# Kernel optimization log

Measured on AMD Instinct MI355X. Metric: run time of the kernel, lower is better.

The kernel has to match this reference:

```python
import jax, jax.numpy as jnp
import numpy as np

C = 512
NUM_GROUPS = 32
EPS = 1e-6


def setup_inputs() -> dict:
    key = jax.random.key(0)
    ks = jax.random.split(key, 10)
    B, H, W = 4, 64, 64
    scale = 1.0 / np.sqrt(C)
    return {
        "hidden_states": jax.random.normal(ks[0], (B, C, H, W), dtype=jnp.float32),
        "gn_scale": jnp.ones((C,), dtype=jnp.float32),
        "gn_bias": jnp.zeros((C,), dtype=jnp.float32),
        "wq": jax.random.normal(ks[1], (C, C), dtype=jnp.float32) * scale,
        "bq": jnp.zeros((C,), dtype=jnp.float32),
        "wk": jax.random.normal(ks[2], (C, C), dtype=jnp.float32) * scale,
        "bk": jnp.zeros((C,), dtype=jnp.float32),
        "wv": jax.random.normal(ks[3], (C, C), dtype=jnp.float32) * scale,
        "bv": jnp.zeros((C,), dtype=jnp.float32),
        "wp": jax.random.normal(ks[4], (C, C), dtype=jnp.float32) * scale,
        "bp": jnp.zeros((C,), dtype=jnp.float32),
    }


def _group_norm(x, scale, bias):
    # x: (B, C, H, W); GroupNorm(32 groups, eps=1e-6, affine)
    B, Cc, H, W = x.shape
    xg = x.reshape(B, NUM_GROUPS, Cc // NUM_GROUPS, H, W)
    mean = jnp.mean(xg, axis=(2, 3, 4), keepdims=True)
    var = jnp.var(xg, axis=(2, 3, 4), keepdims=True)
    xg = (xg - mean) * jax.lax.rsqrt(var + EPS)
    x = xg.reshape(B, Cc, H, W)
    return x * scale[None, :, None, None] + bias[None, :, None, None]


def _conv1x1(x, w, b):
    # 1x1 conv == channel matmul; x: (B,C,H,W), w: (Cout,Cin)
    return jnp.einsum('bchw,oc->bohw', x, w) + b[None, :, None, None]


def reference(hidden_states, gn_scale, gn_bias, wq, bq, wk, bk, wv, bv, wp, bp):
    residual = hidden_states
    h = _group_norm(hidden_states, gn_scale, gn_bias)
    q = _conv1x1(h, wq, bq)
    k = _conv1x1(h, wk, bk)
    v = _conv1x1(h, wv, bv)
    B, Cc, H, W = q.shape
    N = H * W
    q = q.reshape(B, Cc, N)  # (B,C,N)
    k = k.reshape(B, Cc, N)
    v = v.reshape(B, Cc, N)
    # attn[b,i,j] = softmax_j( q_i . k_j * C^-0.5 )
    attn = jnp.einsum('bci,bcj->bij', q, k) * (Cc ** -0.5)
    attn = jax.nn.softmax(attn, axis=2)
    # out[b,c,i] = sum_j v[b,c,j] * attn[b,i,j]
    out = jnp.einsum('bcj,bij->bci', v, attn)
    out = out.reshape(B, Cc, H, W)
    out = _conv1x1(out, wp, bp)
    return out + residual
```

## Files before the change

### kernel.cpp

```cpp
#include <hip/hip_runtime.h>
#include <cstdint>
#include <cstddef>


#define CDIM 512
#define NSP  4096
#define NB   4
#define M0   12.0f

using bf16x8 = __attribute__((ext_vector_type(8))) __bf16;
using f32x4  = __attribute__((ext_vector_type(4))) float;
using u16x4  = __attribute__((ext_vector_type(4))) unsigned short;
using h8     = __attribute__((ext_vector_type(8))) _Float16;

__device__ __forceinline__ unsigned short f2bf(float f) {
  unsigned int u = __float_as_uint(f);
  u += 0x7fffu + ((u >> 16) & 1u);
  return (unsigned short)(u >> 16);
}

__device__ __forceinline__ void async_copy16(const unsigned short* g, unsigned short* l) {
  __builtin_amdgcn_global_load_lds(
      (const __attribute__((address_space(1))) void*)g,
      (__attribute__((address_space(3))) void*)l, 16, 0, 0);
}

__global__ __launch_bounds__(256) void gn_stats(const float* __restrict__ x,
                                                float* __restrict__ stats) {
  const size_t base = (size_t)blockIdx.x * 65536;
  const float4* p = (const float4*)(x + base);
  float s = 0.f, ss = 0.f;
  for (int i = threadIdx.x; i < 16384; i += 256) {
    float4 v = p[i];
    s  += v.x + v.y + v.z + v.w;
    ss += v.x*v.x + v.y*v.y + v.z*v.z + v.w*v.w;
  }
  for (int off = 32; off; off >>= 1) {
    s  += __shfl_xor(s, off);
    ss += __shfl_xor(ss, off);
  }
  __shared__ float rs[4], rss[4];
  const int w = threadIdx.x >> 6;
  if ((threadIdx.x & 63) == 0) { rs[w] = s; rss[w] = ss; }
  __syncthreads();
  if (threadIdx.x == 0) {
    float S  = rs[0] + rs[1] + rs[2] + rs[3];
    float SS = rss[0] + rss[1] + rss[2] + rss[3];
    float mean = S * (1.f / 65536.f);
    float var  = SS * (1.f / 65536.f) - mean * mean;
    stats[2 * blockIdx.x]     = mean;
    stats[2 * blockIdx.x + 1] = rsqrtf(var + 1e-6f);
  }
}

__global__ __launch_bounds__(256) void norm_transpose(
    const float* __restrict__ x, const float* __restrict__ stats,
    const float* __restrict__ gns, const float* __restrict__ gnb,
    unsigned short* __restrict__ hnt) {
  __shared__ float tile[64][65];
  const int b  = blockIdx.z;
  const int c0 = blockIdx.y * 64, n0 = blockIdx.x * 64;
  const int tx = threadIdx.x & 63, ty = threadIdx.x >> 6;
  for (int i = 0; i < 16; ++i) {
    int cl = ty * 16 + i;
    int c  = c0 + cl;
    int g  = c >> 4;
    float mean = stats[(b * 32 + g) * 2];
    float rstd = stats[(b * 32 + g) * 2 + 1];
    float v = x[((size_t)(b * CDIM + c)) * NSP + n0 + tx];
    tile[cl][tx] = (v - mean) * rstd * gns[c] + gnb[c];
  }
  __syncthreads();
  for (int i = 0; i < 16; ++i) {
    int nl = ty * 16 + i;
    hnt[((size_t)(b * NSP + n0 + nl)) * CDIM + c0 + tx] = f2bf(tile[tx][nl]);
  }
}

__global__ __launch_bounds__(256) void weights_to_bf16(
    const float* __restrict__ w0, const float* __restrict__ w1,
    const float* __restrict__ w2, const float* __restrict__ w3,
    unsigned short* __restrict__ o0, unsigned short* __restrict__ o1,
    unsigned short* __restrict__ o2, unsigned short* __restrict__ o3) {
  const float* s; unsigned short* o;
  switch (blockIdx.y) {
    case 0: s = w0; o = o0; break;
    case 1: s = w1; o = o1; break;
    case 2: s = w2; o = o2; break;
    default: s = w3; o = o3; break;
  }
  int i = blockIdx.x * 256 + threadIdx.x;
  float4 v = ((const float4*)s)[i];
  u16x4 r = {f2bf(v.x), f2bf(v.y), f2bf(v.z), f2bf(v.w)};
  *(u16x4*)(o + (size_t)i * 4) = r;
}

template <int BIAS_MODE, int OUT_MODE, int RESID>
__global__ __launch_bounds__(256) void gemm_nt(
    const unsigned short* __restrict__ A, const unsigned short* __restrict__ Bt,
    void* __restrict__ Dv, const float* __restrict__ bias,
    const float* __restrict__ resid,
    int M, int N, int K, float scale, long sA, long sB, long sD, long sR) {
  __shared__ unsigned short lsA[2][128 * 32];
  __shared__ unsigned short lsB[2][128 * 32];
  const int tid = threadIdx.x;
  const int w = tid >> 6, lane = tid & 63;
  const int wr = w >> 1, wc = w & 1;
  const int b = blockIdx.z;
  const int bm0 = blockIdx.y * 128, bn0 = blockIdx.x * 128;
  const unsigned short* Ab = A + (size_t)b * sA;
  const unsigned short* Bb = Bt + (size_t)b * sB;

  f32x4 acc[4][4] = {};
  const int r0  = w * 16 + (lane >> 2);
  const int kof = (lane & 3) * 8;
  const int fr  = lane & 15, kf = (lane >> 4) * 8;

  for (int it = 0; it < 2; ++it) {
    int row = it * 64 + r0;
    async_copy16(Ab + (size_t)(bm0 + row) * K + kof, &lsA[0][row * 32 + kof]);
    async_copy16(Bb + (size_t)(bn0 + row) * K + kof, &lsB[0][row * 32 + kof]);
  }
  __syncthreads();

  int cur = 0;
  for (int k0 = 0; k0 < K; k0 += 32) {
    const int nk = k0 + 32;
    if (nk < K) {
      for (int it = 0; it < 2; ++it) {
        int row = it * 64 + r0;
        async_copy16(Ab + (size_t)(bm0 + row) * K + nk + kof, &lsA[cur ^ 1][row * 32 + kof]);
        async_copy16(Bb + (size_t)(bn0 + row) * K + nk + kof, &lsB[cur ^ 1][row * 32 + kof]);
      }
    }
    bf16x8 af[4], bff[4];
    for (int i = 0; i < 4; ++i) {
      af[i]  = *(const bf16x8*)(&lsA[cur][(wr * 64 + i * 16 + fr) * 32 + kf]);
      bff[i] = *(const bf16x8*)(&lsB[cur][(wc * 64 + i * 16 + fr) * 32 + kf]);
    }
    for (int i = 0; i < 4; ++i)
      for (int j = 0; j < 4; ++j)
        acc[i][j] = __builtin_amdgcn_mfma_f32_16x16x32_bf16(af[i], bff[j], acc[i][j], 0, 0, 0);
    __syncthreads();
    cur ^= 1;
  }

  const int col_l = lane & 15, row_l = (lane >> 4) * 4;
  for (int i = 0; i < 4; ++i)
    for (int j = 0; j < 4; ++j) {
      int gr = bm0 + wr * 64 + i * 16 + row_l;
      int gc = bn0 + wc * 64 + j * 16 + col_l;
      for (int r = 0; r < 4; ++r) {
        float v = acc[i][j][r] * scale;
        if (BIAS_MODE == 1) v += bias[gr + r];
        if (BIAS_MODE == 2) v += bias[gc];
        if (RESID) v += resid[(size_t)b * sR + (size_t)(gr + r) * N + gc];
        if (OUT_MODE == 1)
          ((unsigned short*)Dv)[(size_t)b * sD + (size_t)(gr + r) * N + gc] = f2bf(v);
        else
          ((float*)Dv)[(size_t)b * sD + (size_t)(gr + r) * N + gc] = v;
      }
    }
}

template <int OUT_MODE, int SPLITK, int EXPL, int XSWZ>
__global__ __launch_bounds__(256, 2) void gemm128(
    const unsigned short* __restrict__ A, const unsigned short* __restrict__ Bt,
    void* __restrict__ Dv, float* __restrict__ lsum,
    int M, int N, int K, float scale, long sA, long sB, long sD, int kLen) {
  __shared__ unsigned short lsA[2][128 * 32];
  __shared__ unsigned short lsB[2][128 * 32];
  const int tid = threadIdx.x;
  const int wid = tid >> 6, lane = tid & 63;
  const int wr = wid >> 1, wc = wid & 1;
  const int fr = lane & 15, kq = lane >> 4;
  const int b = SPLITK ? (blockIdx.z & 3) : blockIdx.z;
  int bx = blockIdx.x;
  if (XSWZ) bx = (bx & 7) * (gridDim.x >> 3) + (bx >> 3);
  const int bm0 = blockIdx.y * 128, bn0 = bx * 128;
  const unsigned short* Ab = A + (size_t)b * sA;
  const unsigned short* Bb = Bt + (size_t)b * sB;
  const size_t dOff = SPLITK ? (size_t)blockIdx.z * (size_t)M * N
                             : (size_t)b * (size_t)sD;
  const int kStart = SPLITK ? (blockIdx.z >> 2) * kLen : 0;
  const int ntiles = (SPLITK ? kLen : K) >> 5;

  auto stage = [&](int t, int buf) {
    const int k0 = kStart + t * 32;
    const int sr0 = wid * 32 + (lane >> 2);
    const int c  = lane & 3;
#pragma unroll
    for (int i = 0; i < 2; ++i) {
      const int r = sr0 + i * 16;
      async_copy16(Ab + (size_t)(bm0 + r) * K + k0 + ((c ^ (r & 3)) << 3),
                   &lsA[buf][r * 32 + c * 8]);
    }
#pragma unroll
    for (int i = 0; i < 2; ++i) {
      const int r = sr0 + i * 16;
      async_copy16(Bb + (size_t)(bn0 + r) * K + k0 + ((c ^ (r & 3)) << 3),
                   &lsB[buf][r * 32 + c * 8]);
    }
  };

  f32x4 acc[4][4] = {};
  const int cko  = (kq ^ (fr & 3)) << 3;
  const int arow = wr * 64 + fr;
  const int brow = wc * 64 + fr;

  stage(0, 0);
  for (int t = 0; t < ntiles; ++t) {
    const int cur = t & 1;
    if (t + 1 < ntiles) {
      stage(t + 1, cur ^ 1);
      asm volatile("s_waitcnt vmcnt(4)\n\ts_barrier" ::: "memory");
    } else {
      asm volatile("s_waitcnt vmcnt(0)\n\ts_barrier" ::: "memory");
    }
    bf16x8 af[4], bg[4];
#pragma unroll
    for (int i = 0; i < 4; ++i)
      af[i] = *(const bf16x8*)&lsA[cur][(arow + i * 16) * 32 + cko];
#pragma unroll
    for (int j = 0; j < 4; ++j)
      bg[j] = *(const bf16x8*)&lsB[cur][(brow + j * 16) * 32 + cko];
#pragma unroll
    for (int i = 0; i < 4; ++i)
#pragma unroll
      for (int j = 0; j < 4; ++j)
        acc[i][j] = __builtin_amdgcn_mfma_f32_16x16x32_bf16(af[i], bg[j], acc[i][j], 0, 0, 0);
    asm volatile("s_barrier" ::: "memory");
  }

  float rs[4][4];
  if (EXPL)
#pragma unroll
    for (int i = 0; i < 4; ++i)
#pragma unroll
      for (int r = 0; r < 4; ++r) rs[i][r] = 0.f;

#pragma unroll
  for (int mi = 0; mi < 4; ++mi)
#pragma unroll
    for (int ni = 0; ni < 4; ++ni) {
      const int gr = bm0 + wr * 64 + mi * 16 + kq * 4;
      const int gc = bn0 + wc * 64 + ni * 16 + fr;
#pragma unroll
      for (int r = 0; r < 4; ++r) {
        float v;
        if (EXPL) {
          v = __expf(fmaf(acc[mi][ni][r], scale, -M0));
          rs[mi][r] += v;
        } else {
          v = acc[mi][ni][r] * scale;
        }
        if (OUT_MODE == 1)
          ((unsigned short*)Dv)[dOff + (size_t)(gr + r) * N + gc] = f2bf(v);
        else
          ((_Float16*)Dv)[dOff + (size_t)(gr + r) * N + gc] = (_Float16)v;
      }
    }

  if (EXPL) {
#pragma unroll
    for (int mi = 0; mi < 4; ++mi)
#pragma unroll
      for (int r = 0; r < 4; ++r) {
        float v = rs[mi][r];
        v += __shfl_xor(v, 1); v += __shfl_xor(v, 2);
        v += __shfl_xor(v, 4); v += __shfl_xor(v, 8);
        if (fr == 0) {
          int gr = bm0 + wr * 64 + mi * 16 + kq * 4 + r;
          atomicAdd(&lsum[(size_t)b * M + gr], v);
        }
      }
  }
}

__global__ __launch_bounds__(256) void reduce_div(const _Float16* __restrict__ Op,
                                                  const float* __restrict__ l,
                                                  unsigned short* __restrict__ ot) {
  const size_t stride = (size_t)NB * NSP * CDIM;
  size_t base = ((size_t)blockIdx.x * 256 + threadIdx.x) * 8;
  float linv = 1.f / l[base >> 9];
  h8 a = *(const h8*)(Op + base);
  h8 c = *(const h8*)(Op + stride + base);
  u16x4 o0, o1;
#pragma unroll
  for (int i = 0; i < 4; ++i) {
    o0[i] = f2bf(((float)a[i] + (float)c[i]) * linv);
    o1[i] = f2bf(((float)a[i + 4] + (float)c[i + 4]) * linv);
  }
  *(u16x4*)(ot + base) = o0;
  *(u16x4*)(ot + base + 4) = o1;
}

extern "C" void kernel_launch(void* const* d_in, const int* in_sizes, int n_in,
                              void* d_out, int out_size, void* d_ws, size_t ws_size,
                              hipStream_t stream) {
  const float* hs  = (const float*)d_in[0];
  const float* gns = (const float*)d_in[1];
  const float* gnb = (const float*)d_in[2];
  const float* wq  = (const float*)d_in[3];
  const float* bq  = (const float*)d_in[4];
  const float* wk  = (const float*)d_in[5];
  const float* bk  = (const float*)d_in[6];
  const float* wv  = (const float*)d_in[7];
  const float* bv  = (const float*)d_in[8];
  const float* wp  = (const float*)d_in[9];
  const float* bp  = (const float*)d_in[10];

  char* p = (char*)d_ws;
  unsigned short* wqb = (unsigned short*)p; p += (size_t)CDIM * CDIM * 2;
  unsigned short* wkb = (unsigned short*)p; p += (size_t)CDIM * CDIM * 2;
  unsigned short* wvb = (unsigned short*)p; p += (size_t)CDIM * CDIM * 2;
  unsigned short* wpb = (unsigned short*)p; p += (size_t)CDIM * CDIM * 2;
  const size_t bn = (size_t)NSP * CDIM;
  unsigned short* hnt = (unsigned short*)p; p += NB * bn * 2;
  unsigned short* qt  = (unsigned short*)p; p += NB * bn * 2;
  unsigned short* kt  = (unsigned short*)p; p += NB * bn * 2;
  unsigned short* vcn = (unsigned short*)p; p += NB * bn * 2;
  unsigned short* P   = (unsigned short*)p; p += (size_t)NB * NSP * NSP * 2;
  _Float16* Op = (_Float16*)p;  p += (size_t)2 * NB * bn * 2;
  float* lsum  = (float*)p;     p += (size_t)NB * NSP * 4;
  float* stats = (float*)p;     p += 256 * 4;
  unsigned short* ot = hnt;

  hipMemsetAsync(lsum, 0, (size_t)NB * NSP * 4, stream);
  weights_to_bf16<<<dim3(256, 4), 256, 0, stream>>>(wq, wk, wv, wp, wqb, wkb, wvb, wpb);
  gn_stats<<<128, 256, 0, stream>>>(hs, stats);
  norm_transpose<<<dim3(64, 8, 4), 256, 0, stream>>>(hs, stats, gns, gnb, hnt);

  const long sBN = (long)bn;
  const long sPP = (long)NSP * NSP;
  gemm_nt<2, 1, 0><<<dim3(4, 32, NB), 256, 0, stream>>>(
      hnt, wqb, qt, bq, nullptr, NSP, CDIM, CDIM, 1.f, sBN, 0, sBN, 0);
  gemm_nt<2, 1, 0><<<dim3(4, 32, NB), 256, 0, stream>>>(
      hnt, wkb, kt, bk, nullptr, NSP, CDIM, CDIM, 1.f, sBN, 0, sBN, 0);
  gemm_nt<1, 1, 0><<<dim3(32, 4, NB), 256, 0, stream>>>(
      wvb, hnt, vcn, bv, nullptr, CDIM, NSP, CDIM, 1.f, 0, sBN, sBN, 0);

  const float sc = 0.044194173824159216f;
  gemm128<1, 0, 1, 1><<<dim3(32, 32, NB), 256, 0, stream>>>(
      qt, kt, P, lsum, NSP, NSP, CDIM, sc, sBN, sBN, sPP, 0);

  gemm128<2, 1, 0, 0><<<dim3(4, 32, 2 * NB), 256, 0, stream>>>(
      P, vcn, Op, nullptr, NSP, CDIM, NSP, 1.f, sPP, sBN, 0, NSP / 2);

  reduce_div<<<4096, 256, 0, stream>>>(Op, lsum, ot);

  gemm_nt<1, 0, 1><<<dim3(32, 4, NB), 256, 0, stream>>>(
      wpb, ot, (float*)d_out, bp, hs, CDIM, NSP, CDIM, 1.f, 0, sBN, sBN, sBN);
}
```

Baseline: 367.6 us.

## Enlarge attention GEMM tiles to 256x256 with 16-wave blocks and K=64 staging

Result: faster. 297.5 us (-19.1%).

```diff
diff --git a/kernel.cpp b/kernel.cpp
--- a/kernel.cpp
+++ b/kernel.cpp
@@ -163,50 +163,49 @@
     }
 }
 
-template <int OUT_MODE, int SPLITK, int EXPL, int XSWZ>
-__global__ __launch_bounds__(256, 2) void gemm128(
+template <int OUT_MODE, int SPLITK, int EXPL>
+__global__ __launch_bounds__(1024, 4) void gemm256w(
     const unsigned short* __restrict__ A, const unsigned short* __restrict__ Bt,
     void* __restrict__ Dv, float* __restrict__ lsum,
     int M, int N, int K, float scale, long sA, long sB, long sD, int kLen) {
-  __shared__ unsigned short lsA[2][128 * 32];
-  __shared__ unsigned short lsB[2][128 * 32];
+  __shared__ unsigned short lsA[2][256 * 64];
+  __shared__ unsigned short lsB[2][256 * 64];
   const int tid = threadIdx.x;
   const int wid = tid >> 6, lane = tid & 63;
-  const int wr = wid >> 1, wc = wid & 1;
+  const int wm = wid >> 2, wn = wid & 3;
   const int fr = lane & 15, kq = lane >> 4;
   const int b = SPLITK ? (blockIdx.z & 3) : blockIdx.z;
-  int bx = blockIdx.x;
-  if (XSWZ) bx = (bx & 7) * (gridDim.x >> 3) + (bx >> 3);
-  const int bm0 = blockIdx.y * 128, bn0 = bx * 128;
+  const int bm0 = blockIdx.y * 256, bn0 = blockIdx.x * 256;
   const unsigned short* Ab = A + (size_t)b * sA;
   const unsigned short* Bb = Bt + (size_t)b * sB;
   const size_t dOff = SPLITK ? (size_t)blockIdx.z * (size_t)M * N
                              : (size_t)b * (size_t)sD;
   const int kStart = SPLITK ? (blockIdx.z >> 2) * kLen : 0;
-  const int ntiles = (SPLITK ? kLen : K) >> 5;
+  const int ntiles = (SPLITK ? kLen : K) >> 6;
 
   auto stage = [&](int t, int buf) {
-    const int k0 = kStart + t * 32;
-    const int sr0 = wid * 32 + (lane >> 2);
-    const int c  = lane & 3;
+    const int k0 = kStart + t * 64;
 #pragma unroll
     for (int i = 0; i < 2; ++i) {
-      const int r = sr0 + i * 16;
-      async_copy16(Ab + (size_t)(bm0 + r) * K + k0 + ((c ^ (r & 3)) << 3),
-                   &lsA[buf][r * 32 + c * 8]);
+      const int idx = i * 1024 + tid;
+      const int row = idx >> 3, ch = idx & 7;
+      const int sch = ch ^ (row & 7);
+      async_copy16(Ab + (size_t)(bm0 + row) * K + k0 + sch * 8,
+                   &lsA[buf][row * 64 + ch * 8]);
     }
 #pragma unroll
     for (int i = 0; i < 2; ++i) {
-      const int r = sr0 + i * 16;
-      async_copy16(Bb + (size_t)(bn0 + r) * K + k0 + ((c ^ (r & 3)) << 3),
-                   &lsB[buf][r * 32 + c * 8]);
+      const int idx = i * 1024 + tid;
+      const int row = idx >> 3, ch = idx & 7;
+      const int sch = ch ^ (row & 7);
+      async_copy16(Bb + (size_t)(bn0 + row) * K + k0 + sch * 8,
+                   &lsB[buf][row * 64 + ch * 8]);
     }
   };
 
   f32x4 acc[4][4] = {};
-  const int cko  = (kq ^ (fr & 3)) << 3;
-  const int arow = wr * 64 + fr;
-  const int brow = wc * 64 + fr;
+  const int arow = wm * 64 + fr;
+  const int brow = wn * 64 + fr;
 
   stage(0, 0);
   for (int t = 0; t < ntiles; ++t) {
@@ -217,18 +216,24 @@
     } else {
       asm volatile("s_waitcnt vmcnt(0)\n\ts_barrier" ::: "memory");
     }
-    bf16x8 af[4], bg[4];
-#pragma unroll
-    for (int i = 0; i < 4; ++i)
-      af[i] = *(const bf16x8*)&lsA[cur][(arow + i * 16) * 32 + cko];
-#pragma unroll
-    for (int j = 0; j < 4; ++j)
-      bg[j] = *(const bf16x8*)&lsB[cur][(brow + j * 16) * 32 + cko];
-#pragma unroll
-    for (int i = 0; i < 4; ++i)
+    const unsigned short* la = &lsA[cur][0];
+    const unsigned short* lb = &lsB[cur][0];
+#pragma unroll
+    for (int kh = 0; kh < 2; ++kh) {
+      const int cko = ((kh * 4 + kq) ^ (fr & 7)) * 8;
+      bf16x8 af[4], bg[4];
+#pragma unroll
+      for (int i = 0; i < 4; ++i)
+        af[i] = *(const bf16x8*)&la[(arow + i * 16) * 64 + cko];
 #pragma unroll
       for (int j = 0; j < 4; ++j)
-        acc[i][j] = __builtin_amdgcn_mfma_f32_16x16x32_bf16(af[i], bg[j], acc[i][j], 0, 0, 0);
+        bg[j] = *(const bf16x8*)&lb[(brow + j * 16) * 64 + cko];
+#pragma unroll
+      for (int i = 0; i < 4; ++i)
+#pragma unroll
+        for (int j = 0; j < 4; ++j)
+          acc[i][j] = __builtin_amdgcn_mfma_f32_16x16x32_bf16(af[i], bg[j], acc[i][j], 0, 0, 0);
+    }
     asm volatile("s_barrier" ::: "memory");
   }
 
@@ -243,8 +248,8 @@
   for (int mi = 0; mi < 4; ++mi)
 #pragma unroll
     for (int ni = 0; ni < 4; ++ni) {
-      const int gr = bm0 + wr * 64 + mi * 16 + kq * 4;
-      const int gc = bn0 + wc * 64 + ni * 16 + fr;
+      const int gr = bm0 + wm * 64 + mi * 16 + kq * 4;
+      const int gc = bn0 + wn * 64 + ni * 16 + fr;
 #pragma unroll
       for (int r = 0; r < 4; ++r) {
         float v;
@@ -270,7 +275,7 @@
         v += __shfl_xor(v, 1); v += __shfl_xor(v, 2);
         v += __shfl_xor(v, 4); v += __shfl_xor(v, 8);
         if (fr == 0) {
-          int gr = bm0 + wr * 64 + mi * 16 + kq * 4 + r;
+          int gr = bm0 + wm * 64 + mi * 16 + kq * 4 + r;
           atomicAdd(&lsum[(size_t)b * M + gr], v);
         }
       }
@@ -341,10 +346,10 @@
       wvb, hnt, vcn, bv, nullptr, CDIM, NSP, CDIM, 1.f, 0, sBN, sBN, 0);
 
   const float sc = 0.044194173824159216f;
-  gemm128<1, 0, 1, 1><<<dim3(32, 32, NB), 256, 0, stream>>>(
+  gemm256w<1, 0, 1><<<dim3(16, 16, NB), 1024, 0, stream>>>(
       qt, kt, P, lsum, NSP, NSP, CDIM, sc, sBN, sBN, sPP, 0);
 
-  gemm128<2, 1, 0, 0><<<dim3(4, 32, 2 * NB), 256, 0, stream>>>(
+  gemm256w<2, 1, 0><<<dim3(2, 16, 2 * NB), 1024, 0, stream>>>(
       P, vcn, Op, nullptr, NSP, CDIM, NSP, 1.f, sPP, sBN, 0, NSP / 2);
 
   reduce_div<<<4096, 256, 0, stream>>>(Op, lsum, ot);
```

## Use 256x128 tiles with 512 threads for attention GEMMs and fuse Q/K projections

Applied to the files above, without the earlier changes.

Result: slower. 396.1 us (+7.8%).

```diff
diff --git a/kernel.cpp b/kernel.cpp
--- a/kernel.cpp
+++ b/kernel.cpp
@@ -95,18 +95,21 @@
   *(u16x4*)(o + (size_t)i * 4) = r;
 }
 
-template <int BIAS_MODE, int OUT_MODE, int RESID>
+template <int BIAS_MODE, int OUT_MODE, int RESID, int FUSEQK>
 __global__ __launch_bounds__(256) void gemm_nt(
     const unsigned short* __restrict__ A, const unsigned short* __restrict__ Bt,
     void* __restrict__ Dv, const float* __restrict__ bias,
     const float* __restrict__ resid,
+    const unsigned short* __restrict__ Bt2, void* __restrict__ Dv2,
+    const float* __restrict__ bias2,
     int M, int N, int K, float scale, long sA, long sB, long sD, long sR) {
   __shared__ unsigned short lsA[2][128 * 32];
   __shared__ unsigned short lsB[2][128 * 32];
   const int tid = threadIdx.x;
   const int w = tid >> 6, lane = tid & 63;
   const int wr = w >> 1, wc = w & 1;
-  const int b = blockIdx.z;
+  const int b = FUSEQK ? (blockIdx.z & 3) : blockIdx.z;
+  if (FUSEQK && (blockIdx.z >> 2)) { Bt = Bt2; Dv = Dv2; bias = bias2; }
   const int bm0 = blockIdx.y * 128, bn0 = blockIdx.x * 128;
   const unsigned short* Ab = A + (size_t)b * sA;
   const unsigned short* Bb = Bt + (size_t)b * sB;
@@ -163,21 +166,19 @@
     }
 }
 
-template <int OUT_MODE, int SPLITK, int EXPL, int XSWZ>
-__global__ __launch_bounds__(256, 2) void gemm128(
+template <int OUT_MODE, int SPLITK, int EXPL>
+__global__ __launch_bounds__(512, 4) void gemm512(
     const unsigned short* __restrict__ A, const unsigned short* __restrict__ Bt,
     void* __restrict__ Dv, float* __restrict__ lsum,
     int M, int N, int K, float scale, long sA, long sB, long sD, int kLen) {
-  __shared__ unsigned short lsA[2][128 * 32];
+  __shared__ unsigned short lsA[2][256 * 32];
   __shared__ unsigned short lsB[2][128 * 32];
   const int tid = threadIdx.x;
   const int wid = tid >> 6, lane = tid & 63;
-  const int wr = wid >> 1, wc = wid & 1;
+  const int wm = wid >> 1, wn = wid & 1;
   const int fr = lane & 15, kq = lane >> 4;
   const int b = SPLITK ? (blockIdx.z & 3) : blockIdx.z;
-  int bx = blockIdx.x;
-  if (XSWZ) bx = (bx & 7) * (gridDim.x >> 3) + (bx >> 3);
-  const int bm0 = blockIdx.y * 128, bn0 = bx * 128;
+  const int bm0 = blockIdx.y * 256, bn0 = blockIdx.x * 128;
   const unsigned short* Ab = A + (size_t)b * sA;
   const unsigned short* Bb = Bt + (size_t)b * sB;
   const size_t dOff = SPLITK ? (size_t)blockIdx.z * (size_t)M * N
@@ -187,33 +188,31 @@
 
   auto stage = [&](int t, int buf) {
     const int k0 = kStart + t * 32;
-    const int sr0 = wid * 32 + (lane >> 2);
-    const int c  = lane & 3;
 #pragma unroll
     for (int i = 0; i < 2; ++i) {
-      const int r = sr0 + i * 16;
-      async_copy16(Ab + (size_t)(bm0 + r) * K + k0 + ((c ^ (r & 3)) << 3),
-                   &lsA[buf][r * 32 + c * 8]);
-    }
-#pragma unroll
-    for (int i = 0; i < 2; ++i) {
-      const int r = sr0 + i * 16;
-      async_copy16(Bb + (size_t)(bn0 + r) * K + k0 + ((c ^ (r & 3)) << 3),
-                   &lsB[buf][r * 32 + c * 8]);
+      const int idx = i * 512 + tid;
+      const int row = idx >> 2, ch = idx & 3;
+      async_copy16(Ab + (size_t)(bm0 + row) * K + k0 + ((ch ^ (row & 3)) << 3),
+                   &lsA[buf][row * 32 + ch * 8]);
+    }
+    {
+      const int row = tid >> 2, ch = tid & 3;
+      async_copy16(Bb + (size_t)(bn0 + row) * K + k0 + ((ch ^ (row & 3)) << 3),
+                   &lsB[buf][row * 32 + ch * 8]);
     }
   };
 
   f32x4 acc[4][4] = {};
-  const int cko  = (kq ^ (fr & 3)) << 3;
-  const int arow = wr * 64 + fr;
-  const int brow = wc * 64 + fr;
+  const int cko  = ((kq ^ (fr & 3)) << 3);
+  const int arow = wm * 64 + fr;
+  const int brow = wn * 64 + fr;
 
   stage(0, 0);
   for (int t = 0; t < ntiles; ++t) {
     const int cur = t & 1;
     if (t + 1 < ntiles) {
       stage(t + 1, cur ^ 1);
-      asm volatile("s_waitcnt vmcnt(4)\n\ts_barrier" ::: "memory");
+      asm volatile("s_waitcnt vmcnt(3)\n\ts_barrier" ::: "memory");
     } else {
       asm volatile("s_waitcnt vmcnt(0)\n\ts_barrier" ::: "memory");
     }
@@ -243,8 +242,8 @@
   for (int mi = 0; mi < 4; ++mi)
 #pragma unroll
     for (int ni = 0; ni < 4; ++ni) {
-      const int gr = bm0 + wr * 64 + mi * 16 + kq * 4;
-      const int gc = bn0 + wc * 64 + ni * 16 + fr;
+      const int gr = bm0 + wm * 64 + mi * 16 + kq * 4;
+      const int gc = bn0 + wn * 64 + ni * 16 + fr;
 #pragma unroll
       for (int r = 0; r < 4; ++r) {
         float v;
@@ -270,7 +269,7 @@
         v += __shfl_xor(v, 1); v += __shfl_xor(v, 2);
         v += __shfl_xor(v, 4); v += __shfl_xor(v, 8);
         if (fr == 0) {
-          int gr = bm0 + wr * 64 + mi * 16 + kq * 4 + r;
+          int gr = bm0 + wm * 64 + mi * 16 + kq * 4 + r;
           atomicAdd(&lsum[(size_t)b * M + gr], v);
         }
       }
@@ -333,22 +332,22 @@
 
   const long sBN = (long)bn;
   const long sPP = (long)NSP * NSP;
-  gemm_nt<2, 1, 0><<<dim3(4, 32, NB), 256, 0, stream>>>(
-      hnt, wqb, qt, bq, nullptr, NSP, CDIM, CDIM, 1.f, sBN, 0, sBN, 0);
-  gemm_nt<2, 1, 0><<<dim3(4, 32, NB), 256, 0, stream>>>(
-      hnt, wkb, kt, bk, nullptr, NSP, CDIM, CDIM, 1.f, sBN, 0, sBN, 0);
-  gemm_nt<1, 1, 0><<<dim3(32, 4, NB), 256, 0, stream>>>(
-      wvb, hnt, vcn, bv, nullptr, CDIM, NSP, CDIM, 1.f, 0, sBN, sBN, 0);
+  gemm_nt<2, 1, 0, 1><<<dim3(4, 32, 2 * NB), 256, 0, stream>>>(
+      hnt, wqb, qt, bq, nullptr, wkb, kt, bk, NSP, CDIM, CDIM, 1.f, sBN, 0, sBN, 0);
+  gemm_nt<1, 1, 0, 0><<<dim3(32, 4, NB), 256, 0, stream>>>(
+      wvb, hnt, vcn, bv, nullptr, nullptr, nullptr, nullptr,
+      CDIM, NSP, CDIM, 1.f, 0, sBN, sBN, 0);
 
   const float sc = 0.044194173824159216f;
-  gemm128<1, 0, 1, 1><<<dim3(32, 32, NB), 256, 0, stream>>>(
+  gemm512<1, 0, 1><<<dim3(32, 16, NB), 512, 0, stream>>>(
       qt, kt, P, lsum, NSP, NSP, CDIM, sc, sBN, sBN, sPP, 0);
 
-  gemm128<2, 1, 0, 0><<<dim3(4, 32, 2 * NB), 256, 0, stream>>>(
+  gemm512<2, 1, 0><<<dim3(4, 16, 2 * NB), 512, 0, stream>>>(
       P, vcn, Op, nullptr, NSP, CDIM, NSP, 1.f, sPP, sBN, 0, NSP / 2);
 
   reduce_div<<<4096, 256, 0, stream>>>(Op, lsum, ot);
 
-  gemm_nt<1, 0, 1><<<dim3(32, 4, NB), 256, 0, stream>>>(
-      wpb, ot, (float*)d_out, bp, hs, CDIM, NSP, CDIM, 1.f, 0, sBN, sBN, sBN);
-}
+  gemm_nt<1, 0, 1, 0><<<dim3(32, 4, NB), 256, 0, stream>>>(
+      wpb, ot, (float*)d_out, bp, hs, nullptr, nullptr, nullptr,
+      CDIM, NSP, CDIM, 1.f, 0, sBN, sBN, sBN);
+}
```
